# Performance work log

Hardware: AMD Instinct MI355X
Metric: run time of the kernel (lower is better)

The kernel has to match this reference:

```python
import jax, jax.numpy as jnp
import numpy as np

EMB = 768
HEADS = 12
HEAD_DIM = EMB // HEADS
# Source computes scores / scale with scale = head_dim**-0.5, i.e. scores * sqrt(head_dim)
INV_SCALE = float(HEAD_DIM) ** 0.5


def setup_inputs() -> dict:
    key = jax.random.key(0)
    k1, k2, k3, k4 = jax.random.split(key, 4)
    x = jax.random.normal(k1, (1, 4096, EMB), dtype=jnp.float32)
    qkv_w = jax.random.normal(k2, (3 * EMB, EMB), dtype=jnp.float32) * (EMB ** -0.5)
    out_w = jax.random.normal(k3, (EMB, EMB), dtype=jnp.float32) * (EMB ** -0.5)
    out_b = jax.random.normal(k4, (EMB,), dtype=jnp.float32) * 0.02
    return {"x": x, "qkv_w": qkv_w, "out_w": out_w, "out_b": out_b}


def reference(x, qkv_w, out_w, out_b):
    b, l, d = x.shape
    # qkv: torch Linear (no bias): x @ W^T -> [b, l, 3*d]
    qkv = jnp.einsum('bld,ed->ble', x, qkv_w)
    # rearrange 'b l (n h hd) -> n b h l hd'
    qkv = qkv.reshape(b, l, 3, HEADS, HEAD_DIM).transpose(2, 0, 3, 1, 4)
    q, k, v = qkv[0], qkv[1], qkv[2]
    # scores = (Q K^T) / scale, scale = head_dim**-0.5 => multiply by sqrt(head_dim)
    scores = jnp.einsum('bhqo,bhko->bhqk', q, k) * INV_SCALE
    attn = jax.nn.softmax(scores, axis=-1)  # [b, h, l, l]
    ctx = jnp.einsum('bhqk,bhko->bhqo', attn, v)  # [b, h, l, hd]
    ctx = ctx.transpose(0, 2, 1, 3).reshape(b, l, d)  # 'b h l hd -> b l (h hd)'
    out = jnp.einsum('bld,ed->ble', ctx, out_w) + out_b
    return out
```

## Files before the change

### kernel.cpp

```cpp
#include <hip/hip_runtime.h>

typedef __attribute__((ext_vector_type(8))) short short8;
typedef __attribute__((ext_vector_type(4))) float f32x4;
typedef __attribute__((ext_vector_type(16))) float f32x16;
typedef __attribute__((ext_vector_type(2))) unsigned int uint2v;

#define EMB 768
#define SEQ 4096
#define NH 12
#define HD 64
#define QSCALE 11.541560327111707f

#define GLOBAL_AS __attribute__((address_space(1)))
#define LDS_AS __attribute__((address_space(3)))

__device__ inline ushort f2bf(float v) {
  union { float f; unsigned int u; } x; x.f = v;
  unsigned int r = x.u + 0x7fffu + ((x.u >> 16) & 1u);
  return (ushort)(r >> 16);
}
__device__ inline float bf2f(ushort u) {
  union { float f; unsigned int u32; } x; x.u32 = ((unsigned int)u) << 16;
  return x.f;
}

__device__ inline int cvt_pk_bf16(float a, float b) {
  int r;
  asm("v_cvt_pk_bf16_f32 %0, %1, %2" : "=v"(r) : "v"(a), "v"(b));
  return r;
}
__device__ inline float max3f(float a, float b, float c) {
  float r;
  asm("v_max3_f32 %0, %1, %2, %3" : "=v"(r) : "v"(a), "v"(b), "v"(c));
  return r;
}
__device__ inline void pswap(int& a, int& b) {
  uint2v r = __builtin_amdgcn_permlane32_swap((unsigned)a, (unsigned)b, false, false);
  a = (int)r.x;
  b = (int)r.y;
}

__global__ void split_all(const float* __restrict__ x, const float* __restrict__ qw,
                          const float* __restrict__ ow,
                          ushort* __restrict__ xh, ushort* __restrict__ xl,
                          ushort* __restrict__ qwh, ushort* __restrict__ qwl,
                          ushort* __restrict__ owh, int n14, int n24) {
  int i = blockIdx.x * blockDim.x + threadIdx.x;
  const float4* src;
  ushort4 *dh, *dl;
  int j;
  if (i < n14) {
    src = (const float4*)x; dh = (ushort4*)xh; dl = (ushort4*)xl; j = i;
  } else if (i < n14 + n24) {
    src = (const float4*)qw; dh = (ushort4*)qwh; dl = (ushort4*)qwl; j = i - n14;
  } else {
    j = i - n14 - n24;
    float4 v = ((const float4*)ow)[j];
    ushort4 h = {f2bf(v.x), f2bf(v.y), f2bf(v.z), f2bf(v.w)};
    ((ushort4*)owh)[j] = h;
    return;
  }
  float4 v = src[j];
  ushort4 h = {f2bf(v.x), f2bf(v.y), f2bf(v.z), f2bf(v.w)};
  ushort4 l = {f2bf(v.x - bf2f(h.x)), f2bf(v.y - bf2f(h.y)),
               f2bf(v.z - bf2f(h.z)), f2bf(v.w - bf2f(h.w))};
  dh[j] = h;
  dl[j] = l;
}

__global__ __launch_bounds__(256, 2) void gemm_bt_split(
    const ushort* __restrict__ Ah, const ushort* __restrict__ Al,
    const ushort* __restrict__ Bh, const ushort* __restrict__ Bl,
    int M, int N, int K, int mode,
    float* __restrict__ Cout, const float* __restrict__ bias,
    ushort* __restrict__ Qh, ushort* __restrict__ Ql,
    ushort* __restrict__ Kh, ushort* __restrict__ Kl,
    ushort* __restrict__ Vt) {
  __shared__ ushort smem[2][4 * 128 * 32];

  const int tid = threadIdx.x;
  const int lane = tid & 63;
  const int w = tid >> 6;
  const int wm = w >> 1, wn = w & 1;
  const int col = lane & 15, quad = lane >> 4;
  const int bm = blockIdx.x, bn = blockIdx.y;

  const bool oneterm = (mode == 2) || (mode == 1 && bn >= 12);
  const bool skipdma = oneterm && (w == 1 || w == 3);

  const ushort* gsrc = (w == 0)   ? Ah + (size_t)bm * 128 * K
                       : (w == 1) ? Al + (size_t)bm * 128 * K
                       : (w == 2) ? Bh + (size_t)bn * 128 * K
                                  : Bl + (size_t)bn * 128 * K;
  const int loff = w * 4096;
  const ushort* g0 = gsrc + (size_t)(lane >> 2) * K + (lane & 3) * 8;

  f32x4 acc[4][4];
  const f32x4 zz = {0.f, 0.f, 0.f, 0.f};
#pragma unroll
  for (int i = 0; i < 4; ++i)
#pragma unroll
    for (int j = 0; j < 4; ++j) acc[i][j] = zz;

#define GSTAGE(b, kt)                                                       \
  if (!skipdma) {                                                           \
    _Pragma("unroll") for (int i = 0; i < 8; ++i) {                         \
      __builtin_amdgcn_global_load_lds(                                     \
          (const GLOBAL_AS unsigned int*)(g0 + (size_t)i * 16 * K + (kt)),  \
          (LDS_AS unsigned int*)(&smem[b][loff + i * 512]), 16, 0, 0);      \
    }                                                                       \
  }

  GSTAGE(0, 0);
  const int nk = K / 32;
  for (int it = 0; it < nk; ++it) {
    const int buf = it & 1;
    asm volatile("s_waitcnt vmcnt(0)" ::: "memory");
    __syncthreads();
    if (it + 1 < nk) GSTAGE(buf ^ 1, (it + 1) * 32);

    const ushort* sAh = &smem[buf][0];
    const ushort* sAl = &smem[buf][4096];
    const ushort* sBh = &smem[buf][8192];
    const ushort* sBl = &smem[buf][12288];

    if (oneterm) {
      short8 fah[4], fbh[4];
#pragma unroll
      for (int t = 0; t < 4; ++t) {
        fah[t] = *(const short8*)(&sAh[(wm * 64 + t * 16 + col) * 32 + quad * 8]);
        fbh[t] = *(const short8*)(&sBh[(wn * 64 + t * 16 + col) * 32 + quad * 8]);
      }
#pragma unroll
      for (int tm = 0; tm < 4; ++tm)
#pragma unroll
        for (int tn = 0; tn < 4; ++tn)
          acc[tm][tn] = __builtin_amdgcn_mfma_f32_16x16x32_bf16(fah[tm], fbh[tn], acc[tm][tn], 0, 0, 0);
    } else {
      short8 fah[4], fal[4], fbh[4], fbl[4];
#pragma unroll
      for (int t = 0; t < 4; ++t) {
        int ra = (wm * 64 + t * 16 + col) * 32 + quad * 8;
        fah[t] = *(const short8*)(&sAh[ra]);
        fal[t] = *(const short8*)(&sAl[ra]);
        int rb = (wn * 64 + t * 16 + col) * 32 + quad * 8;
        fbh[t] = *(const short8*)(&sBh[rb]);
        fbl[t] = *(const short8*)(&sBl[rb]);
      }
#pragma unroll
      for (int tm = 0; tm < 4; ++tm)
#pragma unroll
        for (int tn = 0; tn < 4; ++tn) {
          acc[tm][tn] = __builtin_amdgcn_mfma_f32_16x16x32_bf16(fah[tm], fbh[tn], acc[tm][tn], 0, 0, 0);
          acc[tm][tn] = __builtin_amdgcn_mfma_f32_16x16x32_bf16(fah[tm], fbl[tn], acc[tm][tn], 0, 0, 0);
          acc[tm][tn] = __builtin_amdgcn_mfma_f32_16x16x32_bf16(fal[tm], fbh[tn], acc[tm][tn], 0, 0, 0);
        }
    }
  }

  const int m_base = bm * 128 + wm * 64;
  const int n_base = bn * 128 + wn * 64;

  if (mode != 1) {
#pragma unroll
    for (int tm = 0; tm < 4; ++tm)
#pragma unroll
      for (int tn = 0; tn < 4; ++tn) {
        int gn = n_base + tn * 16 + col;
        float b = bias[gn];
#pragma unroll
        for (int rr = 0; rr < 4; ++rr) {
          int gm = m_base + tm * 16 + quad * 4 + rr;
          Cout[(size_t)gm * N + gn] = acc[tm][tn][rr] + b;
        }
      }
  } else {
    int reg = bn / 6;
    if (reg < 2) {
#pragma unroll
      for (int tm = 0; tm < 4; ++tm)
#pragma unroll
        for (int tn = 0; tn < 4; ++tn) {
          int el = (bn % 6) * 128 + wn * 64 + tn * 16 + col;
          int hh = el >> 6, dd = el & 63;
#pragma unroll
          for (int rr = 0; rr < 4; ++rr) {
            int gm = m_base + tm * 16 + quad * 4 + rr;
            float v = acc[tm][tn][rr];
            if (reg == 0) {
              v *= QSCALE;
              ushort hi = f2bf(v);
              size_t idx = ((size_t)hh * SEQ + gm) * HD + dd;
              Qh[idx] = hi;
              Ql[idx] = f2bf(v - bf2f(hi));
            } else {
              ushort hi = f2bf(v);
              int pc = ((dd >> 3) ^ (gm & 7)) & 7;
              size_t idx = ((size_t)hh * SEQ + gm) * HD + pc * 8 + (dd & 7);
              Kh[idx] = hi;
              Kl[idx] = f2bf(v - bf2f(hi));
            }
          }
        }
    } else {
      __syncthreads();
      ushort* vt_tile = &smem[0][0];
#pragma unroll
      for (int tm = 0; tm < 4; ++tm)
#pragma unroll
        for (int tn = 0; tn < 4; ++tn) {
          int el = wn * 64 + tn * 16 + col;
#pragma unroll
          for (int rr = 0; rr < 4; ++rr) {
            int seq = wm * 64 + tm * 16 + quad * 4 + rr;
            int cc = (((seq >> 3) & 7) ^ (el & 7)) & 7;
            vt_tile[el * 128 + (seq & 64) + cc * 8 + (seq & 7)] = f2bf(acc[tm][tn][rr]);
          }
        }
      __syncthreads();
      int el = tid >> 1;
      int elg = (bn % 6) * 128 + el;
      int hh = elg >> 6, dd = elg & 63;
      ushort* grow = Vt + (size_t)(hh * HD + dd) * SEQ + bm * 128;
#pragma unroll
      for (int i = 0; i < 8; ++i) {
        int c = ((tid & 1) * 8 + i + el) & 15;
        *(uint4*)(grow + c * 8) = *(const uint4*)(&vt_tile[el * 128 + c * 8]);
      }
    }
  }
}

__global__ __launch_bounds__(256, 3) void attn_k(
    const ushort* __restrict__ Qh, const ushort* __restrict__ Ql,
    const ushort* __restrict__ Kh, const ushort* __restrict__ Kl,
    const ushort* __restrict__ Vt, ushort* __restrict__ Ch) {
  __shared__ __attribute__((aligned(128))) ushort smem[6 * 4096];

  const int tid = threadIdx.x, lane = tid & 63, w = tid >> 6;
  const int wq = w >> 1, wk = w & 1;
  const int qc = lane & 31, hl = lane >> 5;

  const int lid = blockIdx.x + (int)(gridDim.x) * blockIdx.y;
  const int wid = (lid & 7) * 96 + (lid >> 3);
  const int head = wid >> 6;
  const int qb = (wid & 63) * 64 + wq * 32;

  const ushort* qh_base = Qh + ((size_t)head * SEQ + qb + qc) * HD + hl * 8;
  const ushort* ql_base = Ql + ((size_t)head * SEQ + qb + qc) * HD + hl * 8;
  short8 fqh[4], fql[4];
#pragma unroll
  for (int d = 0; d < 4; ++d) {
    fqh[d] = *(const short8*)(qh_base + d * 16);
    fql[d] = *(const short8*)(ql_base + d * 16);
  }

  const ushort* khg = Kh + (size_t)head * SEQ * HD;
  const ushort* klg = Kl + (size_t)head * SEQ * HD;
  const ushort* vtg = Vt + (size_t)head * HD * SEQ;
  const ushort* gp[6];
  ushort* lp[6];
  int gstep[6];
#pragma unroll
  for (int i = 0; i < 6; ++i) {
    int idx = w * 6 + i;
    int arr = idx >> 3, j = idx & 7;
    if (arr == 0) {
      gp[i] = khg + (size_t)(j * 8 + (lane >> 3)) * 64 + (lane & 7) * 8;
      lp[i] = &smem[0 + j * 512];
      gstep[i] = 64 * 64;
    } else if (arr == 1) {
      gp[i] = klg + (size_t)(j * 8 + (lane >> 3)) * 64 + (lane & 7) * 8;
      lp[i] = &smem[8192 + j * 512];
      gstep[i] = 64 * 64;
    } else {
      gp[i] = vtg + (size_t)(j * 8 + (lane >> 3)) * SEQ + (lane & 7) * 8;
      lp[i] = &smem[16384 + j * 512];
      gstep[i] = 64;
    }
  }
#pragma unroll
  for (int i = 0; i < 6; ++i) {
    __builtin_amdgcn_global_load_lds((const GLOBAL_AS unsigned int*)gp[i],
                                     (LDS_AS unsigned int*)lp[i], 16, 0, 0);
    gp[i] += gstep[i];
  }

  int koff[4];
#pragma unroll
  for (int d = 0; d < 4; ++d)
    koff[d] = ((wk * 32 + qc) * 64 + (((d * 2 + hl) ^ (qc & 7)) & 7) * 8) * 2;
  int voff[2][2];
#pragma unroll
  for (int td = 0; td < 2; ++td)
#pragma unroll
    for (int ks = 0; ks < 2; ++ks)
      voff[td][ks] =
          ((td * 32 + qc) * 64 + (((wk * 4 + ks * 2 + hl) ^ (qc & 7)) & 7) * 8) * 2;

  float m2 = -1e30f, ell = 0.f;
  f32x16 o0, o1;
#pragma unroll
  for (int r = 0; r < 16; ++r) { o0[r] = 0.f; o1[r] = 0.f; }

  auto do_iter = [&](int buf, bool pf) {
    asm volatile("s_waitcnt vmcnt(0)" ::: "memory");
    __syncthreads();
    if (pf) {
#pragma unroll
      for (int i = 0; i < 6; ++i) {
        __builtin_amdgcn_global_load_lds(
            (const GLOBAL_AS unsigned int*)gp[i],
            (LDS_AS unsigned int*)(lp[i] + (buf ^ 1) * 4096), 16, 0, 0);
        gp[i] += gstep[i];
      }
    }
    const char* kh = (const char*)&smem[buf * 4096];
    const char* kl = (const char*)&smem[8192 + buf * 4096];
    const char* vt = (const char*)&smem[16384 + buf * 4096];

    f32x16 s;
#pragma unroll
    for (int r = 0; r < 16; ++r) s[r] = 0.f;
#pragma unroll
    for (int d = 0; d < 4; ++d) {
      short8 akh = *(const short8*)(kh + koff[d]);
      short8 akl = *(const short8*)(kl + koff[d]);
      s = __builtin_amdgcn_mfma_f32_32x32x16_bf16(akh, fqh[d], s, 0, 0, 0);
      s = __builtin_amdgcn_mfma_f32_32x32x16_bf16(akl, fqh[d], s, 0, 0, 0);
      s = __builtin_amdgcn_mfma_f32_32x32x16_bf16(akh, fql[d], s, 0, 0, 0);
    }
    short8 fv00 = *(const short8*)(vt + voff[0][0]);
    short8 fv01 = *(const short8*)(vt + voff[0][1]);
    short8 fv10 = *(const short8*)(vt + voff[1][0]);
    short8 fv11 = *(const short8*)(vt + voff[1][1]);

    float a1 = max3f(s[0], s[1], s[2]);
    float a2 = max3f(s[3], s[4], s[5]);
    float a3 = max3f(s[6], s[7], s[8]);
    float a4 = max3f(s[9], s[10], s[11]);
    float a5 = max3f(s[12], s[13], s[14]);
    float lm = fmaxf(max3f(a1, a2, a3), max3f(a4, a5, s[15]));
    if (!__all(lm <= m2)) {
      float om = __shfl_xor(lm, 32);
      float vm = fmaxf(lm, om);
      float mn = fmaxf(m2, vm + 48.0f);
      float alpha = exp2f(m2 - mn);
      m2 = mn;
      ell *= alpha;
#pragma unroll
      for (int r = 0; r < 16; ++r) { o0[r] *= alpha; o1[r] *= alpha; }
    }
#pragma unroll
    for (int r = 0; r < 16; ++r) s[r] = exp2f(s[r] - m2);
    float ps = (((s[0] + s[1]) + (s[2] + s[3])) + ((s[4] + s[5]) + (s[6] + s[7]))) +
               (((s[8] + s[9]) + (s[10] + s[11])) + ((s[12] + s[13]) + (s[14] + s[15])));
    ell += ps;

    int pk[8];
#pragma unroll
    for (int d = 0; d < 8; ++d) pk[d] = cvt_pk_bf16(s[2 * d], s[2 * d + 1]);
    pswap(pk[0], pk[2]);
    pswap(pk[1], pk[3]);
    pswap(pk[4], pk[6]);
    pswap(pk[5], pk[7]);
    union { int i[4]; short8 s8; } b0, b1;
    b0.i[0] = pk[0]; b0.i[1] = pk[1]; b0.i[2] = pk[2]; b0.i[3] = pk[3];
    b1.i[0] = pk[4]; b1.i[1] = pk[5]; b1.i[2] = pk[6]; b1.i[3] = pk[7];

    o0 = __builtin_amdgcn_mfma_f32_32x32x16_bf16(fv00, b0.s8, o0, 0, 0, 0);
    o0 = __builtin_amdgcn_mfma_f32_32x32x16_bf16(fv01, b1.s8, o0, 0, 0, 0);
    o1 = __builtin_amdgcn_mfma_f32_32x32x16_bf16(fv10, b0.s8, o1, 0, 0, 0);
    o1 = __builtin_amdgcn_mfma_f32_32x32x16_bf16(fv11, b1.s8, o1, 0, 0, 0);
  };

  for (int kb = 0; kb < SEQ - 128; kb += 128) {
    do_iter(0, true);
    do_iter(1, true);
  }
  do_iter(0, true);
  do_iter(1, false);

  ell += __shfl_xor(ell, 32);

  __syncthreads();
  float* ob = (float*)&smem[4096 + wq * 8192];
  float* mel = (float*)&smem[20480];
  if (wk == 1) {
    *(f32x16*)(ob + lane * 32) = o0;
    *(f32x16*)(ob + lane * 32 + 16) = o1;
    mel[wq * 128 + lane] = m2;
    mel[wq * 128 + 64 + lane] = ell;
  }
  __syncthreads();
  if (wk == 0) {
    float m2B = mel[wq * 128 + lane];
    float ellB = mel[wq * 128 + 64 + lane];
    f32x16 p0 = *(const f32x16*)(ob + lane * 32);
    f32x16 p1 = *(const f32x16*)(ob + lane * 32 + 16);
    float mN = fmaxf(m2, m2B);
    float aA = exp2f(m2 - mN), aB = exp2f(m2B - mN);
    float inv = 1.0f / (ell * aA + ellB * aB);
    ushort* crow = Ch + (size_t)(qb + qc) * EMB + head * 64 + hl * 4;
#pragma unroll
    for (int r = 0; r < 8; ++r) {
      int off = ((2 * r) & 3) + 8 * (r >> 1);
      float v0 = (o0[2 * r] * aA + p0[2 * r] * aB) * inv;
      float v1 = (o0[2 * r + 1] * aA + p0[2 * r + 1] * aB) * inv;
      *(unsigned int*)(crow + off) = (unsigned int)cvt_pk_bf16(v0, v1);
      float w0 = (o1[2 * r] * aA + p1[2 * r] * aB) * inv;
      float w1 = (o1[2 * r + 1] * aA + p1[2 * r + 1] * aB) * inv;
      *(unsigned int*)(crow + 32 + off) = (unsigned int)cvt_pk_bf16(w0, w1);
    }
  }
}

extern "C" void kernel_launch(void* const* d_in, const int* in_sizes, int n_in,
                              void* d_out, int out_size, void* d_ws, size_t ws_size,
                              hipStream_t stream) {
  const float* x = (const float*)d_in[0];
  const float* qkv_w = (const float*)d_in[1];
  const float* out_w = (const float*)d_in[2];
  const float* out_b = (const float*)d_in[3];
  float* out = (float*)d_out;

  char* p = (char*)d_ws;
  auto carve = [&](size_t bytes) {
    char* q = p;
    p += (bytes + 255) & ~(size_t)255;
    return q;
  };
  const size_t NX = (size_t)SEQ * EMB;
  const size_t NQW = (size_t)3 * EMB * EMB;
  const size_t NOW = (size_t)EMB * EMB;
  const size_t NQKV = (size_t)NH * SEQ * HD;

  ushort* xh = (ushort*)carve(NX * 2);
  ushort* xl = (ushort*)carve(NX * 2);
  ushort* qwh = (ushort*)carve(NQW * 2);
  ushort* qwl = (ushort*)carve(NQW * 2);
  ushort* owh = (ushort*)carve(NOW * 2);
  ushort* Qh = (ushort*)carve(NQKV * 2);
  ushort* Ql = (ushort*)carve(NQKV * 2);
  ushort* Kh = (ushort*)carve(NQKV * 2);
  ushort* Kl = (ushort*)carve(NQKV * 2);
  ushort* Vt = (ushort*)carve(NQKV * 2);
  ushort* Ch = (ushort*)carve(NX * 2);

  const int ntot4 = (int)((NX + NQW + NOW) / 4);
  split_all<<<dim3(ntot4 / 256), 256, 0, stream>>>(
      x, qkv_w, out_w, xh, xl, qwh, qwl, owh, (int)(NX / 4), (int)(NQW / 4));

  gemm_bt_split<<<dim3(32, 18), 256, 0, stream>>>(
      xh, xl, qwh, qwl, SEQ, 3 * EMB, EMB, 1,
      nullptr, nullptr, Qh, Ql, Kh, Kl, Vt);

  attn_k<<<dim3(SEQ / 64, NH), 256, 0, stream>>>(Qh, Ql, Kh, Kl, Vt, Ch);

  gemm_bt_split<<<dim3(32, 6), 256, 0, stream>>>(
      Ch, Ch, owh, owh, SEQ, EMB, EMB, 2,
      out, out_b, nullptr, nullptr, nullptr, nullptr, nullptr);
}
```

Measured before the change: 198.5 us.

## Load K fragments directly from global into registers instead of LDS staging

The K hi/lo tiles are no longer staged through LDS with async global-to-LDS copies. Each wave now loads its own K MFMA operand fragments straight from global memory into registers, prefetching the next block during the current iteration. The QKV producer writes K unswizzled to match, and LDS use drops to the V tile plus the epilogue buffers. This removes LDS traffic and LDS footprint for K, which could allow more resident blocks. The cost is duplicate global/L2 reads of K across query waves, more registers per thread, and global latency that must now be hidden by the register prefetch.

Result: slower. 270.3 us (+36.2%).

```diff
diff --git a/kernel.cpp b/kernel.cpp
--- a/kernel.cpp
+++ b/kernel.cpp
@@ -187,16 +187,14 @@
           for (int rr = 0; rr < 4; ++rr) {
             int gm = m_base + tm * 16 + quad * 4 + rr;
             float v = acc[tm][tn][rr];
+            size_t idx = ((size_t)hh * SEQ + gm) * HD + dd;
             if (reg == 0) {
               v *= QSCALE;
               ushort hi = f2bf(v);
-              size_t idx = ((size_t)hh * SEQ + gm) * HD + dd;
               Qh[idx] = hi;
               Ql[idx] = f2bf(v - bf2f(hi));
             } else {
               ushort hi = f2bf(v);
-              int pc = ((dd >> 3) ^ (gm & 7)) & 7;
-              size_t idx = ((size_t)hh * SEQ + gm) * HD + pc * 8 + (dd & 7);
               Kh[idx] = hi;
               Kl[idx] = f2bf(v - bf2f(hi));
             }
@@ -235,7 +233,7 @@
     const ushort* __restrict__ Qh, const ushort* __restrict__ Ql,
     const ushort* __restrict__ Kh, const ushort* __restrict__ Kl,
     const ushort* __restrict__ Vt, ushort* __restrict__ Ch) {
-  __shared__ __attribute__((aligned(128))) ushort smem[6 * 4096];
+  __shared__ __attribute__((aligned(128))) ushort smem[8704];
 
   const int tid = threadIdx.x, lane = tid & 63, w = tid >> 6;
   const int wq = w >> 1, wk = w & 1;
@@ -255,41 +253,33 @@
     fql[d] = *(const short8*)(ql_base + d * 16);
   }
 
-  const ushort* khg = Kh + (size_t)head * SEQ * HD;
-  const ushort* klg = Kl + (size_t)head * SEQ * HD;
+  const ushort* kgh = Kh + (size_t)head * SEQ * HD + (size_t)(wk * 32 + qc) * HD + hl * 8;
+  const ushort* kgl = Kl + (size_t)head * SEQ * HD + (size_t)(wk * 32 + qc) * HD + hl * 8;
+  short8 kfh[4], kfl[4];
+#pragma unroll
+  for (int d = 0; d < 4; ++d) {
+    kfh[d] = *(const short8*)(kgh + d * 16);
+    kfl[d] = *(const short8*)(kgl + d * 16);
+  }
+  kgh += 64 * HD;
+  kgl += 64 * HD;
+
   const ushort* vtg = Vt + (size_t)head * HD * SEQ;
-  const ushort* gp[6];
-  ushort* lp[6];
-  int gstep[6];
-#pragma unroll
-  for (int i = 0; i < 6; ++i) {
-    int idx = w * 6 + i;
-    int arr = idx >> 3, j = idx & 7;
-    if (arr == 0) {
-      gp[i] = khg + (size_t)(j * 8 + (lane >> 3)) * 64 + (lane & 7) * 8;
-      lp[i] = &smem[0 + j * 512];
-      gstep[i] = 64 * 64;
-    } else if (arr == 1) {
-      gp[i] = klg + (size_t)(j * 8 + (lane >> 3)) * 64 + (lane & 7) * 8;
-      lp[i] = &smem[8192 + j * 512];
-      gstep[i] = 64 * 64;
-    } else {
-      gp[i] = vtg + (size_t)(j * 8 + (lane >> 3)) * SEQ + (lane & 7) * 8;
-      lp[i] = &smem[16384 + j * 512];
-      gstep[i] = 64;
-    }
-  }
-#pragma unroll
-  for (int i = 0; i < 6; ++i) {
-    __builtin_amdgcn_global_load_lds((const GLOBAL_AS unsigned int*)gp[i],
-                                     (LDS_AS unsigned int*)lp[i], 16, 0, 0);
-    gp[i] += gstep[i];
-  }
-
-  int koff[4];
-#pragma unroll
-  for (int d = 0; d < 4; ++d)
-    koff[d] = ((wk * 32 + qc) * 64 + (((d * 2 + hl) ^ (qc & 7)) & 7) * 8) * 2;
+  const ushort* gpv[2];
+  ushort* lpv[2];
+#pragma unroll
+  for (int i = 0; i < 2; ++i) {
+    int j = w * 2 + i;
+    gpv[i] = vtg + (size_t)(j * 8 + (lane >> 3)) * SEQ + (lane & 7) * 8;
+    lpv[i] = &smem[j * 512];
+  }
+#pragma unroll
+  for (int i = 0; i < 2; ++i) {
+    __builtin_amdgcn_global_load_lds((const GLOBAL_AS unsigned int*)gpv[i],
+                                     (LDS_AS unsigned int*)lpv[i], 16, 0, 0);
+    gpv[i] += 64;
+  }
+
   int voff[2][2];
 #pragma unroll
   for (int td = 0; td < 2; ++td)
@@ -308,32 +298,37 @@
     __syncthreads();
     if (pf) {
 #pragma unroll
-      for (int i = 0; i < 6; ++i) {
+      for (int i = 0; i < 2; ++i) {
         __builtin_amdgcn_global_load_lds(
-            (const GLOBAL_AS unsigned int*)gp[i],
-            (LDS_AS unsigned int*)(lp[i] + (buf ^ 1) * 4096), 16, 0, 0);
-        gp[i] += gstep[i];
-      }
-    }
-    const char* kh = (const char*)&smem[buf * 4096];
-    const char* kl = (const char*)&smem[8192 + buf * 4096];
-    const char* vt = (const char*)&smem[16384 + buf * 4096];
+            (const GLOBAL_AS unsigned int*)gpv[i],
+            (LDS_AS unsigned int*)(lpv[i] + (buf ^ 1) * 4096), 16, 0, 0);
+        gpv[i] += 64;
+      }
+    }
+    const char* vt = (const char*)&smem[buf * 4096];
 
     f32x16 s;
 #pragma unroll
     for (int r = 0; r < 16; ++r) s[r] = 0.f;
 #pragma unroll
     for (int d = 0; d < 4; ++d) {
-      short8 akh = *(const short8*)(kh + koff[d]);
-      short8 akl = *(const short8*)(kl + koff[d]);
-      s = __builtin_amdgcn_mfma_f32_32x32x16_bf16(akh, fqh[d], s, 0, 0, 0);
-      s = __builtin_amdgcn_mfma_f32_32x32x16_bf16(akl, fqh[d], s, 0, 0, 0);
-      s = __builtin_amdgcn_mfma_f32_32x32x16_bf16(akh, fql[d], s, 0, 0, 0);
+      s = __builtin_amdgcn_mfma_f32_32x32x16_bf16(kfh[d], fqh[d], s, 0, 0, 0);
+      s = __builtin_amdgcn_mfma_f32_32x32x16_bf16(kfl[d], fqh[d], s, 0, 0, 0);
+      s = __builtin_amdgcn_mfma_f32_32x32x16_bf16(kfh[d], fql[d], s, 0, 0, 0);
     }
     short8 fv00 = *(const short8*)(vt + voff[0][0]);
     short8 fv01 = *(const short8*)(vt + voff[0][1]);
     short8 fv10 = *(const short8*)(vt + voff[1][0]);
     short8 fv11 = *(const short8*)(vt + voff[1][1]);
+    if (pf) {
+#pragma unroll
+      for (int d = 0; d < 4; ++d) {
+        kfh[d] = *(const short8*)(kgh + d * 16);
+        kfl[d] = *(const short8*)(kgl + d * 16);
+      }
+      kgh += 64 * HD;
+      kgl += 64 * HD;
+    }
 
     float a1 = max3f(s[0], s[1], s[2]);
     float a2 = max3f(s[3], s[4], s[5]);
@@ -384,8 +379,8 @@
   ell += __shfl_xor(ell, 32);
 
   __syncthreads();
-  float* ob = (float*)&smem[4096 + wq * 8192];
-  float* mel = (float*)&smem[20480];
+  float* ob = (float*)&smem[wq * 4096];
+  float* mel = (float*)&smem[8192];
   if (wk == 1) {
     *(f32x16*)(ob + lane * 32) = o0;
     *(f32x16*)(ob + lane * 32 + 16) = o1;
```

## Software-pipeline QK^T of next tile with softmax and PV of current tile

Applied to the files above, without the earlier changes.

Splits the attention inner iteration into a QK^T/V-fragment load stage and a softmax+PV finish stage. The loop is restructured so the score MFMAs for the next key tile are issued before the exponentials and PV MFMAs of the previous tile. The aim is to overlap matrix-core work with the VALU softmax and hide dependency stalls. It costs a second score accumulator and a second set of V fragments held in registers, which raises register pressure and may reduce occupancy.

Result: slower. 378.6 us (+90.8%).

```diff
diff --git a/kernel.cpp b/kernel.cpp
--- a/kernel.cpp
+++ b/kernel.cpp
@@ -290,12 +290,12 @@
 #pragma unroll
   for (int d = 0; d < 4; ++d)
     koff[d] = ((wk * 32 + qc) * 64 + (((d * 2 + hl) ^ (qc & 7)) & 7) * 8) * 2;
-  int voff[2][2];
+  int voff[4];
 #pragma unroll
   for (int td = 0; td < 2; ++td)
 #pragma unroll
     for (int ks = 0; ks < 2; ++ks)
-      voff[td][ks] =
+      voff[td * 2 + ks] =
           ((td * 32 + qc) * 64 + (((wk * 4 + ks * 2 + hl) ^ (qc & 7)) & 7) * 8) * 2;
 
   float m2 = -1e30f, ell = 0.f;
@@ -303,23 +303,20 @@
 #pragma unroll
   for (int r = 0; r < 16; ++r) { o0[r] = 0.f; o1[r] = 0.f; }
 
-  auto do_iter = [&](int buf, bool pf) {
-    asm volatile("s_waitcnt vmcnt(0)" ::: "memory");
-    __syncthreads();
-    if (pf) {
-#pragma unroll
-      for (int i = 0; i < 6; ++i) {
-        __builtin_amdgcn_global_load_lds(
-            (const GLOBAL_AS unsigned int*)gp[i],
-            (LDS_AS unsigned int*)(lp[i] + (buf ^ 1) * 4096), 16, 0, 0);
-        gp[i] += gstep[i];
-      }
-    }
+  auto stage = [&](int db) {
+#pragma unroll
+    for (int i = 0; i < 6; ++i) {
+      __builtin_amdgcn_global_load_lds(
+          (const GLOBAL_AS unsigned int*)gp[i],
+          (LDS_AS unsigned int*)(lp[i] + db * 4096), 16, 0, 0);
+      gp[i] += gstep[i];
+    }
+  };
+
+  auto qkv_tile = [&](int buf, f32x16& s, short8 (&fv)[4]) {
     const char* kh = (const char*)&smem[buf * 4096];
     const char* kl = (const char*)&smem[8192 + buf * 4096];
     const char* vt = (const char*)&smem[16384 + buf * 4096];
-
-    f32x16 s;
 #pragma unroll
     for (int r = 0; r < 16; ++r) s[r] = 0.f;
 #pragma unroll
@@ -330,11 +327,13 @@
       s = __builtin_amdgcn_mfma_f32_32x32x16_bf16(akl, fqh[d], s, 0, 0, 0);
       s = __builtin_amdgcn_mfma_f32_32x32x16_bf16(akh, fql[d], s, 0, 0, 0);
     }
-    short8 fv00 = *(const short8*)(vt + voff[0][0]);
-    short8 fv01 = *(const short8*)(vt + voff[0][1]);
-    short8 fv10 = *(const short8*)(vt + voff[1][0]);
-    short8 fv11 = *(const short8*)(vt + voff[1][1]);
-
+    fv[0] = *(const short8*)(vt + voff[0]);
+    fv[1] = *(const short8*)(vt + voff[1]);
+    fv[2] = *(const short8*)(vt + voff[2]);
+    fv[3] = *(const short8*)(vt + voff[3]);
+  };
+
+  auto finish = [&](f32x16& s, short8 (&fv)[4]) {
     float a1 = max3f(s[0], s[1], s[2]);
     float a2 = max3f(s[3], s[4], s[5]);
     float a3 = max3f(s[6], s[7], s[8]);
@@ -368,18 +367,34 @@
     b0.i[0] = pk[0]; b0.i[1] = pk[1]; b0.i[2] = pk[2]; b0.i[3] = pk[3];
     b1.i[0] = pk[4]; b1.i[1] = pk[5]; b1.i[2] = pk[6]; b1.i[3] = pk[7];
 
-    o0 = __builtin_amdgcn_mfma_f32_32x32x16_bf16(fv00, b0.s8, o0, 0, 0, 0);
-    o0 = __builtin_amdgcn_mfma_f32_32x32x16_bf16(fv01, b1.s8, o0, 0, 0, 0);
-    o1 = __builtin_amdgcn_mfma_f32_32x32x16_bf16(fv10, b0.s8, o1, 0, 0, 0);
-    o1 = __builtin_amdgcn_mfma_f32_32x32x16_bf16(fv11, b1.s8, o1, 0, 0, 0);
+    o0 = __builtin_amdgcn_mfma_f32_32x32x16_bf16(fv[0], b0.s8, o0, 0, 0, 0);
+    o0 = __builtin_amdgcn_mfma_f32_32x32x16_bf16(fv[1], b1.s8, o0, 0, 0, 0);
+    o1 = __builtin_amdgcn_mfma_f32_32x32x16_bf16(fv[2], b0.s8, o1, 0, 0, 0);
+    o1 = __builtin_amdgcn_mfma_f32_32x32x16_bf16(fv[3], b1.s8, o1, 0, 0, 0);
   };
 
-  for (int kb = 0; kb < SEQ - 128; kb += 128) {
-    do_iter(0, true);
-    do_iter(1, true);
-  }
-  do_iter(0, true);
-  do_iter(1, false);
+#define WAITBAR() do { asm volatile("s_waitcnt vmcnt(0)" ::: "memory"); __syncthreads(); } while (0)
+
+  f32x16 sA, sB;
+  short8 fvA[4], fvB[4];
+
+  WAITBAR();
+  stage(1);
+  qkv_tile(0, sA, fvA);
+  for (int i = 0; i < 31; ++i) {
+    WAITBAR();
+    stage(0);
+    qkv_tile(1, sB, fvB);
+    finish(sA, fvA);
+    WAITBAR();
+    stage(1);
+    qkv_tile(0, sA, fvA);
+    finish(sB, fvB);
+  }
+  WAITBAR();
+  qkv_tile(1, sB, fvB);
+  finish(sA, fvA);
+  finish(sB, fvB);
 
   ell += __shfl_xor(ell, 32);
 
```

## Software-pipeline attention loop: overlap next QK^T MFMAs with current softmax and PV

Applied to the files above, without the earlier changes.

Restructures the flash-attention inner loop so the QK^T MFMAs and V-fragment LDS reads for the next key block are issued before the softmax, exp, bf16 packing and PV MFMAs of the current block. Two score accumulators and two sets of V fragments alternate between ping-pong buffers, with explicit prologue and epilogue stages replacing the lambda. The aim is to hide exp/VALU latency behind matrix-core work and to hide LDS latency. In exchange it raises VGPR pressure, which could lower occupancy or cause spills.

Result: slower. 266.1 us (+34.1%).

```diff
diff --git a/kernel.cpp b/kernel.cpp
--- a/kernel.cpp
+++ b/kernel.cpp
@@ -290,96 +290,119 @@
 #pragma unroll
   for (int d = 0; d < 4; ++d)
     koff[d] = ((wk * 32 + qc) * 64 + (((d * 2 + hl) ^ (qc & 7)) & 7) * 8) * 2;
-  int voff[2][2];
-#pragma unroll
-  for (int td = 0; td < 2; ++td)
-#pragma unroll
-    for (int ks = 0; ks < 2; ++ks)
-      voff[td][ks] =
-          ((td * 32 + qc) * 64 + (((wk * 4 + ks * 2 + hl) ^ (qc & 7)) & 7) * 8) * 2;
+  const int voff0 = ((0 * 32 + qc) * 64 + (((wk * 4 + 0 * 2 + hl) ^ (qc & 7)) & 7) * 8) * 2;
+  const int voff1 = ((0 * 32 + qc) * 64 + (((wk * 4 + 1 * 2 + hl) ^ (qc & 7)) & 7) * 8) * 2;
+  const int voff2 = ((1 * 32 + qc) * 64 + (((wk * 4 + 0 * 2 + hl) ^ (qc & 7)) & 7) * 8) * 2;
+  const int voff3 = ((1 * 32 + qc) * 64 + (((wk * 4 + 1 * 2 + hl) ^ (qc & 7)) & 7) * 8) * 2;
 
   float m2 = -1e30f, ell = 0.f;
   f32x16 o0, o1;
 #pragma unroll
   for (int r = 0; r < 16; ++r) { o0[r] = 0.f; o1[r] = 0.f; }
 
-  auto do_iter = [&](int buf, bool pf) {
-    asm volatile("s_waitcnt vmcnt(0)" ::: "memory");
-    __syncthreads();
-    if (pf) {
-#pragma unroll
-      for (int i = 0; i < 6; ++i) {
-        __builtin_amdgcn_global_load_lds(
-            (const GLOBAL_AS unsigned int*)gp[i],
-            (LDS_AS unsigned int*)(lp[i] + (buf ^ 1) * 4096), 16, 0, 0);
-        gp[i] += gstep[i];
-      }
-    }
-    const char* kh = (const char*)&smem[buf * 4096];
-    const char* kl = (const char*)&smem[8192 + buf * 4096];
-    const char* vt = (const char*)&smem[16384 + buf * 4096];
-
-    f32x16 s;
-#pragma unroll
-    for (int r = 0; r < 16; ++r) s[r] = 0.f;
-#pragma unroll
-    for (int d = 0; d < 4; ++d) {
-      short8 akh = *(const short8*)(kh + koff[d]);
-      short8 akl = *(const short8*)(kl + koff[d]);
-      s = __builtin_amdgcn_mfma_f32_32x32x16_bf16(akh, fqh[d], s, 0, 0, 0);
-      s = __builtin_amdgcn_mfma_f32_32x32x16_bf16(akl, fqh[d], s, 0, 0, 0);
-      s = __builtin_amdgcn_mfma_f32_32x32x16_bf16(akh, fql[d], s, 0, 0, 0);
-    }
-    short8 fv00 = *(const short8*)(vt + voff[0][0]);
-    short8 fv01 = *(const short8*)(vt + voff[0][1]);
-    short8 fv10 = *(const short8*)(vt + voff[1][0]);
-    short8 fv11 = *(const short8*)(vt + voff[1][1]);
-
-    float a1 = max3f(s[0], s[1], s[2]);
-    float a2 = max3f(s[3], s[4], s[5]);
-    float a3 = max3f(s[6], s[7], s[8]);
-    float a4 = max3f(s[9], s[10], s[11]);
-    float a5 = max3f(s[12], s[13], s[14]);
-    float lm = fmaxf(max3f(a1, a2, a3), max3f(a4, a5, s[15]));
-    if (!__all(lm <= m2)) {
-      float om = __shfl_xor(lm, 32);
-      float vm = fmaxf(lm, om);
-      float mn = fmaxf(m2, vm + 48.0f);
-      float alpha = exp2f(m2 - mn);
-      m2 = mn;
-      ell *= alpha;
-#pragma unroll
-      for (int r = 0; r < 16; ++r) { o0[r] *= alpha; o1[r] *= alpha; }
-    }
-#pragma unroll
-    for (int r = 0; r < 16; ++r) s[r] = exp2f(s[r] - m2);
-    float ps = (((s[0] + s[1]) + (s[2] + s[3])) + ((s[4] + s[5]) + (s[6] + s[7]))) +
-               (((s[8] + s[9]) + (s[10] + s[11])) + ((s[12] + s[13]) + (s[14] + s[15])));
-    ell += ps;
-
-    int pk[8];
-#pragma unroll
-    for (int d = 0; d < 8; ++d) pk[d] = cvt_pk_bf16(s[2 * d], s[2 * d + 1]);
-    pswap(pk[0], pk[2]);
-    pswap(pk[1], pk[3]);
-    pswap(pk[4], pk[6]);
-    pswap(pk[5], pk[7]);
-    union { int i[4]; short8 s8; } b0, b1;
-    b0.i[0] = pk[0]; b0.i[1] = pk[1]; b0.i[2] = pk[2]; b0.i[3] = pk[3];
-    b1.i[0] = pk[4]; b1.i[1] = pk[5]; b1.i[2] = pk[6]; b1.i[3] = pk[7];
-
-    o0 = __builtin_amdgcn_mfma_f32_32x32x16_bf16(fv00, b0.s8, o0, 0, 0, 0);
-    o0 = __builtin_amdgcn_mfma_f32_32x32x16_bf16(fv01, b1.s8, o0, 0, 0, 0);
-    o1 = __builtin_amdgcn_mfma_f32_32x32x16_bf16(fv10, b0.s8, o1, 0, 0, 0);
-    o1 = __builtin_amdgcn_mfma_f32_32x32x16_bf16(fv11, b1.s8, o1, 0, 0, 0);
-  };
-
-  for (int kb = 0; kb < SEQ - 128; kb += 128) {
-    do_iter(0, true);
-    do_iter(1, true);
-  }
-  do_iter(0, true);
-  do_iter(1, false);
+#define STAGE(db)                                                         \
+  {                                                                       \
+    _Pragma("unroll") for (int i = 0; i < 6; ++i) {                       \
+      __builtin_amdgcn_global_load_lds(                                   \
+          (const GLOBAL_AS unsigned int*)gp[i],                           \
+          (LDS_AS unsigned int*)(lp[i] + (db) * 4096), 16, 0, 0);         \
+      gp[i] += gstep[i];                                                  \
+    }                                                                     \
+  }
+
+#define WAITBAR()                                              \
+  do {                                                         \
+    asm volatile("s_waitcnt vmcnt(0)" ::: "memory");           \
+    __syncthreads();                                           \
+  } while (0)
+
+#define QKVT(bf, s, f0, f1, f2, f3)                                        \
+  {                                                                        \
+    const char* kh = (const char*)&smem[(bf) * 4096];                      \
+    const char* kl = (const char*)&smem[8192 + (bf) * 4096];               \
+    const char* vt = (const char*)&smem[16384 + (bf) * 4096];              \
+    _Pragma("unroll") for (int r = 0; r < 16; ++r) s[r] = 0.f;             \
+    _Pragma("unroll") for (int d = 0; d < 4; ++d) {                        \
+      short8 akh = *(const short8*)(kh + koff[d]);                         \
+      short8 akl = *(const short8*)(kl + koff[d]);                         \
+      s = __builtin_amdgcn_mfma_f32_32x32x16_bf16(akh, fqh[d], s, 0, 0, 0);\
+      s = __builtin_amdgcn_mfma_f32_32x32x16_bf16(akl, fqh[d], s, 0, 0, 0);\
+      s = __builtin_amdgcn_mfma_f32_32x32x16_bf16(akh, fql[d], s, 0, 0, 0);\
+    }                                                                      \
+    f0 = *(const short8*)(vt + voff0);                                     \
+    f1 = *(const short8*)(vt + voff1);                                     \
+    f2 = *(const short8*)(vt + voff2);                                     \
+    f3 = *(const short8*)(vt + voff3);                                     \
+  }
+
+#define FINISH(s, f0, f1, f2, f3)                                          \
+  {                                                                        \
+    float a1 = max3f(s[0], s[1], s[2]);                                    \
+    float a2 = max3f(s[3], s[4], s[5]);                                    \
+    float a3 = max3f(s[6], s[7], s[8]);                                    \
+    float a4 = max3f(s[9], s[10], s[11]);                                  \
+    float a5 = max3f(s[12], s[13], s[14]);                                 \
+    float lm = fmaxf(max3f(a1, a2, a3), max3f(a4, a5, s[15]));             \
+    if (!__all(lm <= m2)) {                                                \
+      float om = __shfl_xor(lm, 32);                                       \
+      float vm = fmaxf(lm, om);                                            \
+      float mn = fmaxf(m2, vm + 48.0f);                                    \
+      float alpha = exp2f(m2 - mn);                                        \
+      m2 = mn;                                                             \
+      ell *= alpha;                                                        \
+      _Pragma("unroll") for (int r = 0; r < 16; ++r) {                     \
+        o0[r] *= alpha;                                                    \
+        o1[r] *= alpha;                                                    \
+      }                                                                    \
+    }                                                                      \
+    _Pragma("unroll") for (int r = 0; r < 16; ++r) s[r] = exp2f(s[r] - m2);\
+    float ps =                                                             \
+        (((s[0] + s[1]) + (s[2] + s[3])) + ((s[4] + s[5]) + (s[6] + s[7])))\
+        + (((s[8] + s[9]) + (s[10] + s[11])) +                             \
+           ((s[12] + s[13]) + (s[14] + s[15])));                           \
+    ell += ps;                                                             \
+    int pk0 = cvt_pk_bf16(s[0], s[1]);                                     \
+    int pk1 = cvt_pk_bf16(s[2], s[3]);                                     \
+    int pk2 = cvt_pk_bf16(s[4], s[5]);                                     \
+    int pk3 = cvt_pk_bf16(s[6], s[7]);                                     \
+    int pk4 = cvt_pk_bf16(s[8], s[9]);                                     \
+    int pk5 = cvt_pk_bf16(s[10], s[11]);                                   \
+    int pk6 = cvt_pk_bf16(s[12], s[13]);                                   \
+    int pk7 = cvt_pk_bf16(s[14], s[15]);                                   \
+    pswap(pk0, pk2);                                                       \
+    pswap(pk1, pk3);                                                       \
+    pswap(pk4, pk6);                                                       \
+    pswap(pk5, pk7);                                                       \
+    union { int i[4]; short8 s8; } b0, b1;                                 \
+    b0.i[0] = pk0; b0.i[1] = pk1; b0.i[2] = pk2; b0.i[3] = pk3;            \
+    b1.i[0] = pk4; b1.i[1] = pk5; b1.i[2] = pk6; b1.i[3] = pk7;            \
+    o0 = __builtin_amdgcn_mfma_f32_32x32x16_bf16(f0, b0.s8, o0, 0, 0, 0);  \
+    o0 = __builtin_amdgcn_mfma_f32_32x32x16_bf16(f1, b1.s8, o0, 0, 0, 0);  \
+    o1 = __builtin_amdgcn_mfma_f32_32x32x16_bf16(f2, b0.s8, o1, 0, 0, 0);  \
+    o1 = __builtin_amdgcn_mfma_f32_32x32x16_bf16(f3, b1.s8, o1, 0, 0, 0);  \
+  }
+
+  f32x16 sA, sB;
+  short8 fvA0, fvA1, fvA2, fvA3;
+  short8 fvB0, fvB1, fvB2, fvB3;
+
+  WAITBAR();
+  STAGE(1);
+  QKVT(0, sA, fvA0, fvA1, fvA2, fvA3);
+  for (int i = 0; i < 31; ++i) {
+    WAITBAR();
+    STAGE(0);
+    QKVT(1, sB, fvB0, fvB1, fvB2, fvB3);
+    FINISH(sA, fvA0, fvA1, fvA2, fvA3);
+    WAITBAR();
+    STAGE(1);
+    QKVT(0, sA, fvA0, fvA1, fvA2, fvA3);
+    FINISH(sB, fvB0, fvB1, fvB2, fvB3);
+  }
+  WAITBAR();
+  QKVT(1, sB, fvB0, fvB1, fvB2, fvB3);
+  FINISH(sA, fvA0, fvA1, fvA2, fvA3);
+  FINISH(sB, fvB0, fvB1, fvB2, fvB3);
 
   ell += __shfl_xor(ell, 32);
 
```
